# Performance work log

Measured on AMD Instinct MI355X. Metric: run time of the kernel, lower is better.

## Reference

```python
import jax, jax.numpy as jnp
import numpy as np

INPUT_DIM = 1024
HIDDEN_DIM = 1024
NUM_HEADS = 16
HEAD_DIM = HIDDEN_DIM // NUM_HEADS


def setup_inputs() -> dict:
    key = jax.random.key(0)
    ks = jax.random.split(key, 11)
    B, S = 2, 2048
    s_in = 1.0 / np.sqrt(INPUT_DIM)
    s_hid = 1.0 / np.sqrt(HIDDEN_DIM)
    return {
        "query": jax.random.normal(ks[0], (B, S, INPUT_DIM), jnp.float32),
        "key": jax.random.normal(ks[1], (B, S, INPUT_DIM), jnp.float32),
        "value": jax.random.normal(ks[2], (B, S, INPUT_DIM), jnp.float32),
        "Wq": jax.random.normal(ks[3], (INPUT_DIM, HIDDEN_DIM), jnp.float32) * s_in,
        "bq": jnp.zeros((HIDDEN_DIM,), jnp.float32),
        "Wk": jax.random.normal(ks[4], (INPUT_DIM, HEAD_DIM), jnp.float32) * s_in,
        "bk": jnp.zeros((HEAD_DIM,), jnp.float32),
        "Wv": jax.random.normal(ks[5], (INPUT_DIM, HEAD_DIM), jnp.float32) * s_in,
        "bv": jnp.zeros((HEAD_DIM,), jnp.float32),
        "Wo": jax.random.normal(ks[6], (HIDDEN_DIM, INPUT_DIM), jnp.float32) * s_hid,
        "bo": jnp.zeros((INPUT_DIM,), jnp.float32),
    }


def reference(query, key, value, Wq, bq, Wk, bk, Wv, bv, Wo, bo):
    B, S, _ = query.shape
    # projections
    q = query @ Wq + bq                       # [B,S,H*D]
    k = key @ Wk + bk                         # [B,S,D]  (single shared head)
    v = value @ Wv + bv                       # [B,S,D]
    q = q.reshape(B, S, NUM_HEADS, HEAD_DIM)  # [B,S,H,D]
    # MQA scores: shared K broadcast over query heads
    scores = jnp.einsum('bqhd,bkd->bhqk', q, k) / np.sqrt(HIDDEN_DIM)
    attn = jax.nn.softmax(scores, axis=-1)    # [B,H,Q,K]
    out = jnp.einsum('bhqk,bkd->bqhd', attn, v)  # [B,Q,H,D]
    out = out.reshape(B, S, HIDDEN_DIM)
    return out @ Wo + bo
```

## Files before the change

### kernel.cpp

```cpp
#include <hip/hip_runtime.h>


typedef unsigned int   u32;
typedef unsigned short u16;
typedef union { float4 v; float f[4]; } f4u;
typedef __attribute__((ext_vector_type(8)))  short frag16;
typedef __attribute__((ext_vector_type(4)))  float f32x4;
typedef __attribute__((ext_vector_type(16))) float f32x16;
typedef union { frag16 v; u32 w[4]; u16 e[8]; } bf8u;

static __device__ __forceinline__ u16 f2bf(float x) {
  union { float f; u32 u; } v; v.f = x;
  u32 r = v.u + 0x7fff + ((v.u >> 16) & 1);
  return (u16)(r >> 16);
}

static __device__ __forceinline__ u32 cvt_pk_bf16(float lo, float hi) {
  u32 r;
  asm("v_cvt_pk_bf16_f32 %0, %1, %2" : "=v"(r) : "v"(lo), "v"(hi));
  return r;
}

static __device__ __forceinline__ void pl32_swap(u32& a, u32& b) {
  asm volatile("v_permlane32_swap_b32 %0, %1" : "+v"(a), "+v"(b));
}

static __device__ __forceinline__ void gload_lds16(const u16* g, u16* l) {
  __builtin_amdgcn_global_load_lds(
      (const __attribute__((address_space(1))) u32*)g,
      (__attribute__((address_space(3))) u32*)l, 16, 0, 0);
}

static __device__ void tcvt_tile(const float* __restrict__ src,
                                 u16* __restrict__ dst,
                                 int C, int ldT, int rt, int ct,
                                 float (*t)[65]) {
  const int r0 = rt * 64, c0 = ct * 64;
  const int tr  = threadIdx.x >> 4;
  const int tc4 = (threadIdx.x & 15) * 4;
#pragma unroll
  for (int i = 0; i < 4; ++i) {
    f4u v; v.v = *(const float4*)(src + (size_t)(r0 + tr + i * 16) * C + c0 + tc4);
    t[tr + i * 16][tc4 + 0] = v.f[0];
    t[tr + i * 16][tc4 + 1] = v.f[1];
    t[tr + i * 16][tc4 + 2] = v.f[2];
    t[tr + i * 16][tc4 + 3] = v.f[3];
  }
  __syncthreads();
#pragma unroll
  for (int i = 0; i < 4; ++i) {
    const int oc = tr + i * 16;
    ushort4 o;
    o.x = f2bf(t[tc4 + 0][oc]);
    o.y = f2bf(t[tc4 + 1][oc]);
    o.z = f2bf(t[tc4 + 2][oc]);
    o.w = f2bf(t[tc4 + 3][oc]);
    *(ushort4*)(dst + (size_t)(c0 + oc) * ldT + r0 + tc4) = o;
  }
}

__global__ __launch_bounds__(256)
void prep_w(const float* __restrict__ Wq, const float* __restrict__ Wo,
            const float* __restrict__ Wk, const float* __restrict__ Wv,
            const float* __restrict__ query,
            u16* __restrict__ wq_t, u16* __restrict__ wo_t,
            u16* __restrict__ wk_t, u16* __restrict__ wv_t,
            u16* __restrict__ xq_bf) {
  const int bid = blockIdx.x;
  if (bid >= 544) {
    const size_t base = (size_t)(bid - 544) * 4096 + threadIdx.x * 16;
    f4u x0, x1, x2, x3;
    x0.v = *(const float4*)(query + base);
    x1.v = *(const float4*)(query + base + 4);
    x2.v = *(const float4*)(query + base + 8);
    x3.v = *(const float4*)(query + base + 12);
    bf8u t0, t1;
    t0.w[0] = cvt_pk_bf16(x0.f[0], x0.f[1]);
    t0.w[1] = cvt_pk_bf16(x0.f[2], x0.f[3]);
    t0.w[2] = cvt_pk_bf16(x1.f[0], x1.f[1]);
    t0.w[3] = cvt_pk_bf16(x1.f[2], x1.f[3]);
    t1.w[0] = cvt_pk_bf16(x2.f[0], x2.f[1]);
    t1.w[1] = cvt_pk_bf16(x2.f[2], x2.f[3]);
    t1.w[2] = cvt_pk_bf16(x3.f[0], x3.f[1]);
    t1.w[3] = cvt_pk_bf16(x3.f[2], x3.f[3]);
    *(frag16*)(xq_bf + base)     = t0.v;
    *(frag16*)(xq_bf + base + 8) = t1.v;
    return;
  }
  __shared__ float t[64][65];
  if (bid < 256)      tcvt_tile(Wq, wq_t, 1024, 1024, bid >> 4, bid & 15, t);
  else if (bid < 512) tcvt_tile(Wo, wo_t, 1024, 1024, (bid - 256) >> 4, (bid - 256) & 15, t);
  else if (bid < 528) tcvt_tile(Wk, wk_t, 64, 1024, bid - 512, 0, t);
  else                tcvt_tile(Wv, wv_t, 64, 1024, bid - 528, 0, t);
}

static __device__ void gemm128n64(const u16* __restrict__ Abf,
                                  const u16* __restrict__ Bt,
                                  const float* __restrict__ bias,
                                  void* __restrict__ Cout, int out_mode,
                                  float oscale, int row0, int col0,
                                  int N, int K, u16* As, u16* Bs) {
  const int tid  = threadIdx.x;
  const int lane = tid & 63;
  const int quad = lane >> 4, l15 = lane & 15;
  const int w = tid >> 6, wy = w >> 1, wx = w & 1;
  const int lrow = lane >> 3, lcol = (lane & 7) * 8;

  f32x4 acc[4][2];
#pragma unroll
  for (int i = 0; i < 4; ++i)
#pragma unroll
    for (int j = 0; j < 2; ++j) {
      acc[i][j][0] = 0.f; acc[i][j][1] = 0.f;
      acc[i][j][2] = 0.f; acc[i][j][3] = 0.f;
    }

  const u16* ag = Abf + (size_t)(row0 + w * 32 + lrow) * K + lcol;
  const u16* bg = Bt  + (size_t)(col0 + w * 16 + lrow) * K + lcol;
  u16* alds = As + w * 4 * 512;
  u16* blds = Bs + w * 2 * 512;

  for (int k0 = 0; k0 < K; k0 += 64) {
    __syncthreads();
#pragma unroll
    for (int i = 0; i < 4; ++i)
      gload_lds16(ag + (size_t)i * 8 * K + k0, alds + i * 512);
#pragma unroll
    for (int i = 0; i < 2; ++i)
      gload_lds16(bg + (size_t)i * 8 * K + k0, blds + i * 512);
    __syncthreads();
#pragma unroll
    for (int ks = 0; ks < 2; ++ks) {
      frag16 af[4], bfr[2];
#pragma unroll
      for (int i = 0; i < 4; ++i)
        af[i] = *(const frag16*)(&As[(wy * 64 + i * 16 + l15) * 64 + ks * 32 + quad * 8]);
#pragma unroll
      for (int j = 0; j < 2; ++j)
        bfr[j] = *(const frag16*)(&Bs[(wx * 32 + j * 16 + l15) * 64 + ks * 32 + quad * 8]);
#pragma unroll
      for (int i = 0; i < 4; ++i)
#pragma unroll
        for (int j = 0; j < 2; ++j)
          acc[i][j] = __builtin_amdgcn_mfma_f32_16x16x32_bf16(af[i], bfr[j], acc[i][j], 0, 0, 0);
    }
  }

  float bj[2];
#pragma unroll
  for (int j = 0; j < 2; ++j)
    bj[j] = bias[col0 + wx * 32 + j * 16 + l15];

#pragma unroll
  for (int i = 0; i < 4; ++i)
#pragma unroll
    for (int rr = 0; rr < 4; ++rr) {
      const size_t row = row0 + wy * 64 + i * 16 + quad * 4 + rr;
#pragma unroll
      for (int j = 0; j < 2; ++j) {
        const float v = (acc[i][j][rr] + bj[j]) * oscale;
        const int col = col0 + wx * 32 + j * 16 + l15;
        if (out_mode == 0) ((float*)Cout)[row * N + col] = v;
        else               ((u16*)Cout)[row * N + col] = f2bf(v);
      }
    }
}

#define GP 72
template <bool A_FP32>
static __device__ void gemm64(const float* __restrict__ Af32,
                              const u16* __restrict__ Abf,
                              const u16* __restrict__ Bt,
                              const float* __restrict__ bias,
                              void* __restrict__ Cout, int out_mode,
                              float oscale,
                              int row0, int col0, int N, int K, int ldT,
                              u16* As, u16* Bs) {
  const int tid  = threadIdx.x;
  const int lane = tid & 63;
  const int quad = lane >> 4, l15 = lane & 15;
  const int w = tid >> 6, wy = w >> 1, wx = w & 1;

  f32x4 acc[2][2];
#pragma unroll
  for (int i = 0; i < 2; ++i)
#pragma unroll
    for (int j = 0; j < 2; ++j) {
      acc[i][j][0] = 0.f; acc[i][j][1] = 0.f;
      acc[i][j][2] = 0.f; acc[i][j][3] = 0.f;
    }

  const int r = tid >> 2, c16 = (tid & 3) * 16;

  for (int k0 = 0; k0 < K; k0 += 64) {
    frag16 a0, a1;
    if (A_FP32) {
      const float* ap = Af32 + (size_t)(row0 + r) * K + k0 + c16;
      f4u x0, x1, x2, x3;
      x0.v = *(const float4*)(ap);
      x1.v = *(const float4*)(ap + 4);
      x2.v = *(const float4*)(ap + 8);
      x3.v = *(const float4*)(ap + 12);
      bf8u t0, t1;
      t0.w[0] = cvt_pk_bf16(x0.f[0], x0.f[1]);
      t0.w[1] = cvt_pk_bf16(x0.f[2], x0.f[3]);
      t0.w[2] = cvt_pk_bf16(x1.f[0], x1.f[1]);
      t0.w[3] = cvt_pk_bf16(x1.f[2], x1.f[3]);
      t1.w[0] = cvt_pk_bf16(x2.f[0], x2.f[1]);
      t1.w[1] = cvt_pk_bf16(x2.f[2], x2.f[3]);
      t1.w[2] = cvt_pk_bf16(x3.f[0], x3.f[1]);
      t1.w[3] = cvt_pk_bf16(x3.f[2], x3.f[3]);
      a0 = t0.v; a1 = t1.v;
    } else {
      const u16* ap = Abf + (size_t)(row0 + r) * K + k0 + c16;
      a0 = *(const frag16*)(ap);
      a1 = *(const frag16*)(ap + 8);
    }
    const u16* bp = Bt + (size_t)(col0 + r) * K + k0 + c16;
    const frag16 b0 = *(const frag16*)(bp);
    const frag16 b1 = *(const frag16*)(bp + 8);
    __syncthreads();
    *(frag16*)(&As[r * GP + c16])     = a0;
    *(frag16*)(&As[r * GP + c16 + 8]) = a1;
    *(frag16*)(&Bs[r * GP + c16])     = b0;
    *(frag16*)(&Bs[r * GP + c16 + 8]) = b1;
    __syncthreads();
#pragma unroll
    for (int ks = 0; ks < 2; ++ks) {
      frag16 af[2], bf[2];
#pragma unroll
      for (int i = 0; i < 2; ++i)
        af[i] = *(const frag16*)(&As[(wy * 32 + i * 16 + l15) * GP + ks * 32 + quad * 8]);
#pragma unroll
      for (int j = 0; j < 2; ++j)
        bf[j] = *(const frag16*)(&Bs[(wx * 32 + j * 16 + l15) * GP + ks * 32 + quad * 8]);
#pragma unroll
      for (int i = 0; i < 2; ++i)
#pragma unroll
        for (int j = 0; j < 2; ++j)
          acc[i][j] = __builtin_amdgcn_mfma_f32_16x16x32_bf16(af[i], bf[j], acc[i][j], 0, 0, 0);
    }
  }

  float bj[2];
#pragma unroll
  for (int j = 0; j < 2; ++j)
    bj[j] = bias[col0 + wx * 32 + j * 16 + l15];

#pragma unroll
  for (int i = 0; i < 2; ++i) {
#pragma unroll
    for (int rr = 0; rr < 4; ++rr) {
      const size_t row = row0 + wy * 32 + i * 16 + quad * 4 + rr;
#pragma unroll
      for (int j = 0; j < 2; ++j) {
        const float v = (acc[i][j][rr] + bj[j]) * oscale;
        const int col = col0 + wx * 32 + j * 16 + l15;
        if (out_mode == 0)      ((float*)Cout)[row * N + col] = v;
        else if (out_mode == 1) ((u16*)Cout)[row * N + col] = f2bf(v);
        else                    ((u16*)Cout)[(size_t)col * ldT + row] = f2bf(v);
      }
    }
  }
}

#define C2_SCALE 0.045084220027780106f

__global__ __launch_bounds__(256, 4)
void proj2(const float* __restrict__ key, const float* __restrict__ value,
           const u16* __restrict__ xq_bf,
           const u16* __restrict__ wq_t, const u16* __restrict__ wk_t,
           const u16* __restrict__ wv_t,
           const float* __restrict__ bq, const float* __restrict__ bk,
           const float* __restrict__ bv,
           u16* __restrict__ q_bf, u16* __restrict__ k_bf,
           u16* __restrict__ vt_bf, int M, int K) {
  __shared__ __align__(16) u16 smem[12288];
  const int bid = blockIdx.x;
  if (bid < 512)
    gemm128n64(xq_bf, wq_t, bq, q_bf, 1, C2_SCALE,
               (bid >> 4) * 128, (bid & 15) * 64, 1024, K, smem, smem + 8192);
  else if (bid < 576)
    gemm64<true>(key, nullptr, wk_t, bk, k_bf, 1, 1.0f,
                 (bid - 512) * 64, 0, 64, K, 0, smem, smem + 64 * GP);
  else
    gemm64<true>(value, nullptr, wv_t, bv, vt_bf, 2, 1.0f,
                 (bid - 576) * 64, 0, 64, K, M, smem, smem + 64 * GP);
}

__global__ __launch_bounds__(256, 4)
void out_proj(const u16* __restrict__ ao, const u16* __restrict__ wo_t,
              const float* __restrict__ bo, float* __restrict__ out,
              int M, int K) {
  __shared__ __align__(16) u16 smem[12288];
  const int bid = blockIdx.x;
  gemm128n64(ao, wo_t, bo, out, 0, 1.0f,
             (bid >> 4) * 128, (bid & 15) * 64, 1024, K, smem, smem + 8192);
}

#define PP 72

__global__ __launch_bounds__(256, 2)
void mqa_flash_mfma(const u16* __restrict__ Qb,
                    const u16* __restrict__ Kb,
                    const u16* __restrict__ Vt,
                    u16* __restrict__ O) {
  const int S = 2048, HID = 1024, D = 64, BS = 4096;
  __shared__ __align__(16) u16 Kss[64 * PP];
  __shared__ __align__(16) u16 Vss[64 * PP];
  __shared__ float lred[4][32];

  const int tid  = threadIdx.x;
  const int lane = tid & 63;
  const int w    = tid >> 6;
  const int l31  = lane & 31;
  const int hh   = lane >> 5;
  const int qb = blockIdx.x, hg = blockIdx.y, b = blockIdx.z;
  const int h = hg * 4 + w;

  const int sr = tid >> 3;
  const int sc = (tid & 7) * 8;

  const u16* kfb0 = &Kss[l31 * PP + hh * 8];
  const u16* kfb1 = &Kss[(32 + l31) * PP + hh * 8];
  const u16* vfb0 = &Vss[l31 * PP + hh * 8];
  const u16* vfb1 = &Vss[(32 + l31) * PP + hh * 8];
  u16* kw0 = &Kss[sr * PP + sc];
  u16* kw1 = &Kss[(sr + 32) * PP + sc];
  u16* vw0 = &Vss[sr * PP + sc];
  u16* vw1 = &Vss[(sr + 32) * PP + sc];

  const u16* qrow = Qb + (size_t)(b * S + qb * 32 + l31) * HID + h * D;
  frag16 qf[4];
#pragma unroll
  for (int ks = 0; ks < 4; ++ks)
    qf[ks] = *(const frag16*)(qrow + ks * 16 + hh * 8);

  f32x16 zero16;
#pragma unroll
  for (int r = 0; r < 16; ++r) zero16[r] = 0.f;
  f32x16 oa0, oa1;
#pragma unroll
  for (int r = 0; r < 16; ++r) { oa0[r] = 0.f; oa1[r] = 0.f; }
  float l_lane = 0.f;

  const u16* kbase = Kb + (size_t)(b * S) * D;
  const u16* vbase = Vt + (size_t)(b * S);

  frag16 pk0 = *(const frag16*)(kbase + (size_t)sr * D + sc);
  frag16 pk1 = *(const frag16*)(kbase + (size_t)(sr + 32) * D + sc);
  frag16 pv0 = *(const frag16*)(vbase + (size_t)sr * BS + sc);
  frag16 pv1 = *(const frag16*)(vbase + (size_t)(sr + 32) * BS + sc);
  *(frag16*)kw0 = pk0;
  *(frag16*)kw1 = pk1;
  *(frag16*)vw0 = pv0;
  *(frag16*)vw1 = pv1;
  pk0 = *(const frag16*)(kbase + (size_t)(64 + sr) * D + sc);
  pk1 = *(const frag16*)(kbase + (size_t)(64 + sr + 32) * D + sc);
  pv0 = *(const frag16*)(vbase + (size_t)sr * BS + 64 + sc);
  pv1 = *(const frag16*)(vbase + (size_t)(sr + 32) * BS + 64 + sc);
  __syncthreads();

  for (int kc = 0; kc < S; kc += 64) {
    frag16 kf0[4], kf1[4], vf0[4], vf1[4];
#pragma unroll
    for (int ks = 0; ks < 4; ++ks) {
      kf0[ks] = *(const frag16*)(kfb0 + ks * 16);
      kf1[ks] = *(const frag16*)(kfb1 + ks * 16);
      vf0[ks] = *(const frag16*)(vfb0 + ks * 16);
      vf1[ks] = *(const frag16*)(vfb1 + ks * 16);
    }
    __syncthreads();

    *(frag16*)kw0 = pk0;
    *(frag16*)kw1 = pk1;
    *(frag16*)vw0 = pv0;
    *(frag16*)vw1 = pv1;

    const int nc = (kc + 128 < S) ? kc + 128 : (S - 64);
    pk0 = *(const frag16*)(kbase + (size_t)(nc + sr) * D + sc);
    pk1 = *(const frag16*)(kbase + (size_t)(nc + sr + 32) * D + sc);
    pv0 = *(const frag16*)(vbase + (size_t)sr * BS + nc + sc);
    pv1 = *(const frag16*)(vbase + (size_t)(sr + 32) * BS + nc + sc);

    f32x16 sa0, sa1;
#pragma unroll
    for (int ks = 0; ks < 4; ++ks)
      sa0 = __builtin_amdgcn_mfma_f32_32x32x16_bf16(kf0[ks], qf[ks], ks ? sa0 : zero16, 0, 0, 0);
#pragma unroll
    for (int ks = 0; ks < 4; ++ks)
      sa1 = __builtin_amdgcn_mfma_f32_32x32x16_bf16(kf1[ks], qf[ks], ks ? sa1 : zero16, 0, 0, 0);

    u32 c0[4], c1[4], d0[4], d1[4];
#pragma unroll
    for (int g = 0; g < 4; ++g) {
      const float p0 = __builtin_amdgcn_exp2f(sa0[g * 4 + 0]);
      const float p1 = __builtin_amdgcn_exp2f(sa0[g * 4 + 1]);
      const float p2 = __builtin_amdgcn_exp2f(sa0[g * 4 + 2]);
      const float p3 = __builtin_amdgcn_exp2f(sa0[g * 4 + 3]);
      const float q0 = __builtin_amdgcn_exp2f(sa1[g * 4 + 0]);
      const float q1 = __builtin_amdgcn_exp2f(sa1[g * 4 + 1]);
      const float q2 = __builtin_amdgcn_exp2f(sa1[g * 4 + 2]);
      const float q3 = __builtin_amdgcn_exp2f(sa1[g * 4 + 3]);
      l_lane += ((p0 + p1) + (p2 + p3)) + ((q0 + q1) + (q2 + q3));
      c0[g] = cvt_pk_bf16(p0, p1); c1[g] = cvt_pk_bf16(p2, p3);
      d0[g] = cvt_pk_bf16(q0, q1); d1[g] = cvt_pk_bf16(q2, q3);
    }

    bf8u pa[4];
    pl32_swap(c0[0], c0[1]); pa[0].w[0] = c0[0]; pa[0].w[2] = c0[1];
    pl32_swap(c1[0], c1[1]); pa[0].w[1] = c1[0]; pa[0].w[3] = c1[1];
    pl32_swap(c0[2], c0[3]); pa[1].w[0] = c0[2]; pa[1].w[2] = c0[3];
    pl32_swap(c1[2], c1[3]); pa[1].w[1] = c1[2]; pa[1].w[3] = c1[3];
    pl32_swap(d0[0], d0[1]); pa[2].w[0] = d0[0]; pa[2].w[2] = d0[1];
    pl32_swap(d1[0], d1[1]); pa[2].w[1] = d1[0]; pa[2].w[3] = d1[1];
    pl32_swap(d0[2], d0[3]); pa[3].w[0] = d0[2]; pa[3].w[2] = d0[3];
    pl32_swap(d1[2], d1[3]); pa[3].w[1] = d1[2]; pa[3].w[3] = d1[3];

#pragma unroll
    for (int ks = 0; ks < 4; ++ks) {
      oa0 = __builtin_amdgcn_mfma_f32_32x32x16_bf16(pa[ks].v, vf0[ks], oa0, 0, 0, 0);
      oa1 = __builtin_amdgcn_mfma_f32_32x32x16_bf16(pa[ks].v, vf1[ks], oa1, 0, 0, 0);
    }

    __syncthreads();
  }

  l_lane += __shfl_xor(l_lane, 32);
  lred[w][l31] = l_lane;

#pragma unroll
  for (int g2 = 0; g2 < 4; ++g2) {
    const f32x4 lv = *(const f32x4*)(&lred[w][g2 * 8 + hh * 4]);
#pragma unroll
    for (int m = 0; m < 4; ++m) {
      const int r = g2 * 4 + m;
      const int q_local = g2 * 8 + hh * 4 + m;
      const float li = 1.f / lv[m];
      u16* orow = O + (size_t)(b * S + qb * 32 + q_local) * HID + h * D;
      orow[l31]      = f2bf(oa0[r] * li);
      orow[32 + l31] = f2bf(oa1[r] * li);
    }
  }
}

extern "C" void kernel_launch(void* const* d_in, const int* in_sizes, int n_in,
                              void* d_out, int out_size, void* d_ws, size_t ws_size,
                              hipStream_t stream) {
  const float* query = (const float*)d_in[0];
  const float* key   = (const float*)d_in[1];
  const float* value = (const float*)d_in[2];
  const float* Wq    = (const float*)d_in[3];
  const float* bq    = (const float*)d_in[4];
  const float* Wk    = (const float*)d_in[5];
  const float* bk    = (const float*)d_in[6];
  const float* Wv    = (const float*)d_in[7];
  const float* bv    = (const float*)d_in[8];
  const float* Wo    = (const float*)d_in[9];
  const float* bo    = (const float*)d_in[10];
  float* out = (float*)d_out;

  const int B = 2, S = 2048, IN = 1024, HID = 1024, H = 16, D = 64;
  const int M = B * S;
  const size_t MB = 1024 * 1024;

  char* ws = (char*)d_ws;
  u16* q_bf  = (u16*)ws;
  u16* ao_bf = (u16*)(ws + 8 * MB);
  u16* xq_bf = ao_bf;
  u16* k_bf  = (u16*)(ws + 16 * MB);
  u16* vt_bf = (u16*)(ws + 16 * MB + 512 * 1024);
  u16* wq_t  = (u16*)(ws + 17 * MB);
  u16* wo_t  = (u16*)(ws + 19 * MB);
  u16* wk_t  = (u16*)(ws + 21 * MB);
  u16* wv_t  = (u16*)(ws + 21 * MB + 128 * 1024);

  dim3 blk(256);
  prep_w<<<dim3(1568), blk, 0, stream>>>(Wq, Wo, Wk, Wv, query,
                                         wq_t, wo_t, wk_t, wv_t, xq_bf);
  proj2<<<dim3(640), blk, 0, stream>>>(key, value, xq_bf, wq_t, wk_t, wv_t,
                                       bq, bk, bv, q_bf, k_bf, vt_bf, M, IN);
  mqa_flash_mfma<<<dim3(S / 32, H / 4, B), blk, 0, stream>>>(q_bf, k_bf, vt_bf, ao_bf);
  out_proj<<<dim3(512), blk, 0, stream>>>(ao_bf, wo_t, bo, out, M, HID);
}
```

Baseline: 201.9 us.

## Use 512-thread attention blocks covering eight heads per shared K/V tile

The attention kernel now launches 512 threads (8 waves) per block, each wave handling one query head, so a single K/V tile in shared memory serves eight heads instead of four. With twice as many threads, each thread stages one row of K and one of V rather than two, which halves per-thread global loads and prefetch registers. The grid halves along the head-group dimension. In exchange, blocks are larger with launch bounds of 1 block per SM hint, so there may be fewer independent blocks for latency hiding, and barriers now synchronise more waves.

New measurement: 197.8 us. 1.02x faster.

```diff
diff --git a/kernel.cpp b/kernel.cpp
--- a/kernel.cpp
+++ b/kernel.cpp
@@ -300,7 +300,7 @@
 
 #define PP 72
 
-__global__ __launch_bounds__(256, 2)
+__global__ __launch_bounds__(512, 1)
 void mqa_flash_mfma(const u16* __restrict__ Qb,
                     const u16* __restrict__ Kb,
                     const u16* __restrict__ Vt,
@@ -308,7 +308,7 @@
   const int S = 2048, HID = 1024, D = 64, BS = 4096;
   __shared__ __align__(16) u16 Kss[64 * PP];
   __shared__ __align__(16) u16 Vss[64 * PP];
-  __shared__ float lred[4][32];
+  __shared__ float lred[8][32];
 
   const int tid  = threadIdx.x;
   const int lane = tid & 63;
@@ -316,7 +316,7 @@
   const int l31  = lane & 31;
   const int hh   = lane >> 5;
   const int qb = blockIdx.x, hg = blockIdx.y, b = blockIdx.z;
-  const int h = hg * 4 + w;
+  const int h = hg * 8 + w;
 
   const int sr = tid >> 3;
   const int sc = (tid & 7) * 8;
@@ -325,10 +325,8 @@
   const u16* kfb1 = &Kss[(32 + l31) * PP + hh * 8];
   const u16* vfb0 = &Vss[l31 * PP + hh * 8];
   const u16* vfb1 = &Vss[(32 + l31) * PP + hh * 8];
-  u16* kw0 = &Kss[sr * PP + sc];
-  u16* kw1 = &Kss[(sr + 32) * PP + sc];
-  u16* vw0 = &Vss[sr * PP + sc];
-  u16* vw1 = &Vss[(sr + 32) * PP + sc];
+  u16* kw = &Kss[sr * PP + sc];
+  u16* vw = &Vss[sr * PP + sc];
 
   const u16* qrow = Qb + (size_t)(b * S + qb * 32 + l31) * HID + h * D;
   frag16 qf[4];
@@ -347,18 +345,12 @@
   const u16* kbase = Kb + (size_t)(b * S) * D;
   const u16* vbase = Vt + (size_t)(b * S);
 
-  frag16 pk0 = *(const frag16*)(kbase + (size_t)sr * D + sc);
-  frag16 pk1 = *(const frag16*)(kbase + (size_t)(sr + 32) * D + sc);
-  frag16 pv0 = *(const frag16*)(vbase + (size_t)sr * BS + sc);
-  frag16 pv1 = *(const frag16*)(vbase + (size_t)(sr + 32) * BS + sc);
-  *(frag16*)kw0 = pk0;
-  *(frag16*)kw1 = pk1;
-  *(frag16*)vw0 = pv0;
-  *(frag16*)vw1 = pv1;
-  pk0 = *(const frag16*)(kbase + (size_t)(64 + sr) * D + sc);
-  pk1 = *(const frag16*)(kbase + (size_t)(64 + sr + 32) * D + sc);
-  pv0 = *(const frag16*)(vbase + (size_t)sr * BS + 64 + sc);
-  pv1 = *(const frag16*)(vbase + (size_t)(sr + 32) * BS + 64 + sc);
+  frag16 pk = *(const frag16*)(kbase + (size_t)sr * D + sc);
+  frag16 pv = *(const frag16*)(vbase + (size_t)sr * BS + sc);
+  *(frag16*)kw = pk;
+  *(frag16*)vw = pv;
+  pk = *(const frag16*)(kbase + (size_t)(64 + sr) * D + sc);
+  pv = *(const frag16*)(vbase + (size_t)sr * BS + 64 + sc);
   __syncthreads();
 
   for (int kc = 0; kc < S; kc += 64) {
@@ -372,16 +364,12 @@
     }
     __syncthreads();
 
-    *(frag16*)kw0 = pk0;
-    *(frag16*)kw1 = pk1;
-    *(frag16*)vw0 = pv0;
-    *(frag16*)vw1 = pv1;
+    *(frag16*)kw = pk;
+    *(frag16*)vw = pv;
 
     const int nc = (kc + 128 < S) ? kc + 128 : (S - 64);
-    pk0 = *(const frag16*)(kbase + (size_t)(nc + sr) * D + sc);
-    pk1 = *(const frag16*)(kbase + (size_t)(nc + sr + 32) * D + sc);
-    pv0 = *(const frag16*)(vbase + (size_t)sr * BS + nc + sc);
-    pv1 = *(const frag16*)(vbase + (size_t)(sr + 32) * BS + nc + sc);
+    pk = *(const frag16*)(kbase + (size_t)(nc + sr) * D + sc);
+    pv = *(const frag16*)(vbase + (size_t)sr * BS + nc + sc);
 
     f32x16 sa0, sa1;
 #pragma unroll
@@ -480,6 +468,6 @@
                                          wq_t, wo_t, wk_t, wv_t, xq_bf);
   proj2<<<dim3(640), blk, 0, stream>>>(key, value, xq_bf, wq_t, wk_t, wv_t,
                                        bq, bk, bv, q_bf, k_bf, vt_bf, M, IN);
-  mqa_flash_mfma<<<dim3(S / 32, H / 4, B), blk, 0, stream>>>(q_bf, k_bf, vt_bf, ao_bf);
+  mqa_flash_mfma<<<dim3(S / 32, H / 8, B), dim3(512), 0, stream>>>(q_bf, k_bf, vt_bf, ao_bf);
   out_proj<<<dim3(512), blk, 0, stream>>>(ao_bf, wo_t, bo, out, M, HID);
 }
```
